# Performance work log

Hardware: AMD Instinct MI355X
Metric: run time of the kernel (lower is better)

## Reference

```python
import jax, jax.numpy as jnp
import numpy as np

EPS = 1e-12  # F.normalize eps

def _l2norm(x, axis=-1):
    n = jnp.sqrt(jnp.sum(x * x, axis=axis, keepdims=True))
    return x / jnp.maximum(n, EPS)

def setup_inputs() -> dict:
    key = jax.random.key(0)
    k1, k2 = jax.random.split(key)
    N, D, C = 262144, 128, 1024
    embeddings = jax.random.normal(k1, (N, D), dtype=jnp.float32)
    labels = jax.random.randint(k2, (N,), 0, C, dtype=jnp.int64)
    return {"embeddings": embeddings, "labels": labels, "num_classes": C}

def reference(embeddings, labels, num_classes):
    # Normalize all embeddings: [N, D]
    emb = _l2norm(embeddings, axis=1)
    # Per-class segment sums and counts (replaces python loop over unique labels)
    sums = jax.ops.segment_sum(emb, labels, num_segments=num_classes)          # [C, D]
    counts = jax.ops.segment_sum(jnp.ones((emb.shape[0],), emb.dtype), labels,
                                 num_segments=num_classes)                     # [C]
    safe_counts = jnp.maximum(counts, 1.0)
    prototypes = _l2norm(sums / safe_counts[:, None], axis=1)                  # [C, D]
    # cosine sim of each sample to its class prototype
    sim = jnp.sum(emb * prototypes[labels], axis=1)                           # [N]
    # per-class mean of (1 - sim)
    loss_sums = jax.ops.segment_sum(1.0 - sim, labels, num_segments=num_classes)
    per_class = loss_sums / safe_counts                                        # [C]
    valid = (counts >= 2.0).astype(emb.dtype)                                  # classes with >=2 samples
    n_valid = jnp.sum(valid)
    loss = jnp.sum(per_class * valid) / jnp.maximum(n_valid, 1.0)
    return jnp.where(n_valid > 0, loss, jnp.zeros((), emb.dtype))
```

## Files before the change

kernel.cpp:

```cpp
#include <hip/hip_runtime.h>
#include <math.h>

#define NUM_CLASSES 1024
#define HIST_CHUNK 2048
#define NB 128

__device__ __forceinline__ int detect_mode32(const int* __restrict__ l) {
    return (l[1] | l[3] | l[5] | l[7] | l[9] | l[11] | l[13] | l[15]) != 0;
}

__device__ __forceinline__ int get_label(const int* __restrict__ l, int i, int mode32) {
    return l[mode32 ? i : (i << 1)] & (NUM_CLASSES - 1);
}

__global__ void hist_kernel(const int* __restrict__ labels, int n,
                            int* __restrict__ pT) {
    __shared__ int h[NUM_CLASSES];
    const int mode32 = detect_mode32(labels);
    for (int i = threadIdx.x; i < NUM_CLASSES; i += blockDim.x) h[i] = 0;
    __syncthreads();
    const int base = blockIdx.x * HIST_CHUNK;
    for (int k = threadIdx.x; k < HIST_CHUNK; k += blockDim.x) {
        int i = base + k;
        if (i < n) atomicAdd(&h[get_label(labels, i, mode32)], 1);
    }
    __syncthreads();
    for (int c = threadIdx.x; c < NUM_CLASSES; c += blockDim.x)
        pT[c * NB + blockIdx.x] = h[c];
}

__global__ __launch_bounds__(512) void scanA_kernel(int* __restrict__ pT,
                                                    int* __restrict__ totals) {
    const int wave = threadIdx.x >> 6;
    const int lane = threadIdx.x & 63;
    const int c = blockIdx.x * 8 + wave;
    int* p = pT + c * NB;
    const int v0 = p[2 * lane];
    const int v1 = p[2 * lane + 1];
    int s = v0 + v1;
    #pragma unroll
    for (int d = 1; d < 64; d <<= 1) {
        int t = __shfl_up(s, d, 64);
        if (lane >= d) s += t;
    }
    const int base = s - v0 - v1;
    p[2 * lane]     = base;
    p[2 * lane + 1] = base + v0;
    if (lane == 63) totals[c] = s;
}

__global__ void scanB_kernel(const int* __restrict__ totals,
                             int* __restrict__ offsets,
                             int* __restrict__ counts,
                             float* __restrict__ accum,
                             int* __restrict__ ticket) {
    __shared__ int tmp[NUM_CLASSES];
    const int c = threadIdx.x;
    const int v = totals[c];
    tmp[c] = v;
    __syncthreads();
    for (int off = 1; off < NUM_CLASSES; off <<= 1) {
        int add = (c >= off) ? tmp[c - off] : 0;
        __syncthreads();
        tmp[c] += add;
        __syncthreads();
    }
    offsets[c] = tmp[c] - v;
    counts[c]  = v;
    if (c == 0) { accum[0] = 0.0f; accum[1] = 0.0f; *ticket = 0; }
}

__global__ void scatter_kernel(const int* __restrict__ labels, int n,
                               const int* __restrict__ pT,
                               const int* __restrict__ offsets,
                               int* __restrict__ sorted) {
    __shared__ int cur[NUM_CLASSES];
    const int mode32 = detect_mode32(labels);
    for (int c = threadIdx.x; c < NUM_CLASSES; c += blockDim.x)
        cur[c] = offsets[c] + pT[c * NB + blockIdx.x];
    __syncthreads();
    const int base = blockIdx.x * HIST_CHUNK;
    for (int k = threadIdx.x; k < HIST_CHUNK; k += blockDim.x) {
        int i = base + k;
        if (i < n) {
            int pos = atomicAdd(&cur[get_label(labels, i, mode32)], 1);
            sorted[pos] = i;
        }
    }
}

#define WPB 8
__global__ __launch_bounds__(512) void class_sum_kernel(
        const float* __restrict__ emb,
        const int* __restrict__ sorted,
        const int* __restrict__ offsets,
        const int* __restrict__ counts,
        float* __restrict__ accum,
        int* __restrict__ ticket,
        float* __restrict__ out) {
    const int c     = blockIdx.x;
    const int start = offsets[c];
    const int count = counts[c];
    const int wave  = threadIdx.x >> 6;
    const int lane  = threadIdx.x & 63;
    const int g     = lane >> 4;
    const int sub   = lane & 15;

    float4 aLo = make_float4(0.f, 0.f, 0.f, 0.f);
    float4 aHi = make_float4(0.f, 0.f, 0.f, 0.f);

    for (int r = wave * 4 + g; r < count; r += WPB * 4) {
        const int idx = sorted[start + r];
        const float4* row = (const float4*)(emb + (size_t)idx * 128);
        float4 v0 = row[sub];
        float4 v1 = row[sub + 16];
        float sq = v0.x*v0.x + v0.y*v0.y + v0.z*v0.z + v0.w*v0.w
                 + v1.x*v1.x + v1.y*v1.y + v1.z*v1.z + v1.w*v1.w;
        sq += __shfl_xor(sq, 1, 64);
        sq += __shfl_xor(sq, 2, 64);
        sq += __shfl_xor(sq, 4, 64);
        sq += __shfl_xor(sq, 8, 64);
        float inv = 1.0f / fmaxf(sqrtf(sq), 1e-12f);
        aLo.x += v0.x * inv; aLo.y += v0.y * inv; aLo.z += v0.z * inv; aLo.w += v0.w * inv;
        aHi.x += v1.x * inv; aHi.y += v1.y * inv; aHi.z += v1.z * inv; aHi.w += v1.w * inv;
    }

    __shared__ float s[WPB * 4][16][8];
    {
        float* dst = s[wave * 4 + g][sub];
        dst[0] = aLo.x; dst[1] = aLo.y; dst[2] = aLo.z; dst[3] = aLo.w;
        dst[4] = aHi.x; dst[5] = aHi.y; dst[6] = aHi.z; dst[7] = aHi.w;
    }
    __syncthreads();

    __shared__ float red[128];
    if (threadIdx.x < 128) {
        const int d  = threadIdx.x;
        const int dd = d & 63;
        const int sb = dd >> 2;
        const int j  = (d >> 6) * 4 + (dd & 3);
        float t = 0.0f;
        #pragma unroll
        for (int k = 0; k < WPB * 4; k++) t += s[k][sb][j];
        red[d] = t * t;
    }
    __syncthreads();
    if (threadIdx.x < 64) {
        float x = red[threadIdx.x] + red[threadIdx.x + 64];
        #pragma unroll
        for (int off = 32; off; off >>= 1) x += __shfl_xor(x, off, 64);
        if (threadIdx.x == 0) {
            if (count >= 2) {
                float nrm = sqrtf(x);
                float per_class = ((float)count - nrm) / (float)count;
                atomicAdd(&accum[0], per_class);
                atomicAdd(&accum[1], 1.0f);
            }
            __threadfence();
            int old = atomicAdd(ticket, 1);
            if (old == NUM_CLASSES - 1) {
                float ls = atomicAdd(&accum[0], 0.0f);
                float nv = atomicAdd(&accum[1], 0.0f);
                out[0] = (nv > 0.0f) ? (ls / nv) : 0.0f;
            }
        }
    }
}

extern "C" void kernel_launch(void* const* d_in, const int* in_sizes, int n_in,
                              void* d_out, int out_size, void* d_ws, size_t ws_size,
                              hipStream_t stream) {
    const float* emb  = (const float*)d_in[0];
    const int* labels = (const int*)d_in[1];
    const int n = in_sizes[1];

    char* ws = (char*)d_ws;
    int*   counts  = (int*)(ws + 0);
    int*   offsets = (int*)(ws + 4096);
    int*   totals  = (int*)(ws + 8192);
    float* accum   = (float*)(ws + 12288);
    int*   ticket  = (int*)(ws + 12304);
    int*   sorted  = (int*)(ws + 16384);
    int*   pT      = (int*)(ws + 16384 + (size_t)n * 4);

    hist_kernel <<<NB, 256, 0, stream>>>(labels, n, pT);
    scanA_kernel<<<NB, 512, 0, stream>>>(pT, totals);
    scanB_kernel<<<1, NUM_CLASSES, 0, stream>>>(totals, offsets, counts, accum, ticket);
    scatter_kernel<<<NB, 256, 0, stream>>>(labels, n, pT, offsets, sorted);
    class_sum_kernel<<<NUM_CLASSES, 512, 0, stream>>>(emb, sorted, offsets, counts,
                                                      accum, ticket, (float*)d_out);
}
```

Baseline: 255.5 us.

## Normalize rows in streaming pass and scatter bf16 copies into class-sorted buffer

The per-class gather of random fp32 rows is replaced by a coalesced streaming pass that normalizes each row and writes a bf16-packed copy to its class-sorted position. The class-sum kernel then reads contiguous half-size rows. This removes scattered full-row reads, but adds an extra write and read of a compacted buffer plus an extra launch. Rounding to bf16 before summing loses precision in the prototype sums.

```diff
diff --git a/kernel.cpp b/kernel.cpp
--- a/kernel.cpp
+++ b/kernel.cpp
@@ -8,10 +8,18 @@
 __device__ __forceinline__ int detect_mode32(const int* __restrict__ l) {
     return (l[1] | l[3] | l[5] | l[7] | l[9] | l[11] | l[13] | l[15]) != 0;
 }
-
 __device__ __forceinline__ int get_label(const int* __restrict__ l, int i, int mode32) {
     return l[mode32 ? i : (i << 1)] & (NUM_CLASSES - 1);
 }
+__device__ __forceinline__ unsigned bf16rne(float x) {
+    unsigned u = __float_as_uint(x);
+    return (u + 0x7FFFu + ((u >> 16) & 1u)) >> 16;
+}
+__device__ __forceinline__ unsigned packbf(float a, float b) {
+    return bf16rne(a) | (bf16rne(b) << 16);
+}
+__device__ __forceinline__ float unpack_lo(unsigned u) { return __uint_as_float(u << 16); }
+__device__ __forceinline__ float unpack_hi(unsigned u) { return __uint_as_float(u & 0xffff0000u); }
 
 __global__ void hist_kernel(const int* __restrict__ labels, int n,
                             int* __restrict__ pT) {
@@ -70,10 +78,10 @@
     if (c == 0) { accum[0] = 0.0f; accum[1] = 0.0f; *ticket = 0; }
 }
 
-__global__ void scatter_kernel(const int* __restrict__ labels, int n,
-                               const int* __restrict__ pT,
-                               const int* __restrict__ offsets,
-                               int* __restrict__ sorted) {
+__global__ void rank_kernel(const int* __restrict__ labels, int n,
+                            const int* __restrict__ pT,
+                            const int* __restrict__ offsets,
+                            int* __restrict__ rank) {
     __shared__ int cur[NUM_CLASSES];
     const int mode32 = detect_mode32(labels);
     for (int c = threadIdx.x; c < NUM_CLASSES; c += blockDim.x)
@@ -82,17 +90,49 @@
     const int base = blockIdx.x * HIST_CHUNK;
     for (int k = threadIdx.x; k < HIST_CHUNK; k += blockDim.x) {
         int i = base + k;
-        if (i < n) {
-            int pos = atomicAdd(&cur[get_label(labels, i, mode32)], 1);
-            sorted[pos] = i;
+        if (i < n)
+            rank[i] = atomicAdd(&cur[get_label(labels, i, mode32)], 1);
+    }
+}
+
+__global__ __launch_bounds__(512) void norm_scatter_kernel(
+        const float* __restrict__ emb,
+        const int* __restrict__ rank,
+        uint4* __restrict__ nbuf,
+        int n) {
+    const int wave = threadIdx.x >> 6;
+    const int lane = threadIdx.x & 63;
+    const int g    = lane >> 4;
+    const int sub  = lane & 15;
+    const int base = blockIdx.x * 256;
+
+    for (int r = wave * 4 + g; r < 256; r += 32) {
+        const int row = base + r;
+        if (row < n) {
+            const float4* rp = (const float4*)(emb + (size_t)row * 128);
+            float4 v0 = rp[sub];
+            float4 v1 = rp[sub + 16];
+            float sq = v0.x*v0.x + v0.y*v0.y + v0.z*v0.z + v0.w*v0.w
+                     + v1.x*v1.x + v1.y*v1.y + v1.z*v1.z + v1.w*v1.w;
+            sq += __shfl_xor(sq, 1, 64);
+            sq += __shfl_xor(sq, 2, 64);
+            sq += __shfl_xor(sq, 4, 64);
+            sq += __shfl_xor(sq, 8, 64);
+            float inv = 1.0f / fmaxf(sqrtf(sq), 1e-12f);
+            uint4 w;
+            w.x = packbf(v0.x * inv, v0.y * inv);
+            w.y = packbf(v0.z * inv, v0.w * inv);
+            w.z = packbf(v1.x * inv, v1.y * inv);
+            w.w = packbf(v1.z * inv, v1.w * inv);
+            const int pos = rank[row];
+            nbuf[(size_t)pos * 16 + sub] = w;
         }
     }
 }
 
 #define WPB 8
-__global__ __launch_bounds__(512) void class_sum_kernel(
-        const float* __restrict__ emb,
-        const int* __restrict__ sorted,
+__global__ __launch_bounds__(512) void class_sum2_kernel(
+        const uint4* __restrict__ nbuf,
         const int* __restrict__ offsets,
         const int* __restrict__ counts,
         float* __restrict__ accum,
@@ -106,39 +146,31 @@
     const int g     = lane >> 4;
     const int sub   = lane & 15;
 
-    float4 aLo = make_float4(0.f, 0.f, 0.f, 0.f);
-    float4 aHi = make_float4(0.f, 0.f, 0.f, 0.f);
+    float a[8];
+    #pragma unroll
+    for (int j = 0; j < 8; j++) a[j] = 0.0f;
 
     for (int r = wave * 4 + g; r < count; r += WPB * 4) {
-        const int idx = sorted[start + r];
-        const float4* row = (const float4*)(emb + (size_t)idx * 128);
-        float4 v0 = row[sub];
-        float4 v1 = row[sub + 16];
-        float sq = v0.x*v0.x + v0.y*v0.y + v0.z*v0.z + v0.w*v0.w
-                 + v1.x*v1.x + v1.y*v1.y + v1.z*v1.z + v1.w*v1.w;
-        sq += __shfl_xor(sq, 1, 64);
-        sq += __shfl_xor(sq, 2, 64);
-        sq += __shfl_xor(sq, 4, 64);
-        sq += __shfl_xor(sq, 8, 64);
-        float inv = 1.0f / fmaxf(sqrtf(sq), 1e-12f);
-        aLo.x += v0.x * inv; aLo.y += v0.y * inv; aLo.z += v0.z * inv; aLo.w += v0.w * inv;
-        aHi.x += v1.x * inv; aHi.y += v1.y * inv; aHi.z += v1.z * inv; aHi.w += v1.w * inv;
+        const uint4 w = nbuf[(size_t)(start + r) * 16 + sub];
+        a[0] += unpack_lo(w.x); a[1] += unpack_hi(w.x);
+        a[2] += unpack_lo(w.y); a[3] += unpack_hi(w.y);
+        a[4] += unpack_lo(w.z); a[5] += unpack_hi(w.z);
+        a[6] += unpack_lo(w.w); a[7] += unpack_hi(w.w);
     }
 
     __shared__ float s[WPB * 4][16][8];
     {
         float* dst = s[wave * 4 + g][sub];
-        dst[0] = aLo.x; dst[1] = aLo.y; dst[2] = aLo.z; dst[3] = aLo.w;
-        dst[4] = aHi.x; dst[5] = aHi.y; dst[6] = aHi.z; dst[7] = aHi.w;
+        #pragma unroll
+        for (int j = 0; j < 8; j++) dst[j] = a[j];
     }
     __syncthreads();
 
     __shared__ float red[128];
     if (threadIdx.x < 128) {
         const int d  = threadIdx.x;
-        const int dd = d & 63;
-        const int sb = dd >> 2;
-        const int j  = (d >> 6) * 4 + (dd & 3);
+        const int sb = d >> 3;
+        const int j  = d & 7;
         float t = 0.0f;
         #pragma unroll
         for (int k = 0; k < WPB * 4; k++) t += s[k][sb][j];
@@ -180,13 +212,17 @@
     int*   totals  = (int*)(ws + 8192);
     float* accum   = (float*)(ws + 12288);
     int*   ticket  = (int*)(ws + 12304);
-    int*   sorted  = (int*)(ws + 16384);
+    int*   rank    = (int*)(ws + 16384);
     int*   pT      = (int*)(ws + 16384 + (size_t)n * 4);
+    uint4* nbuf    = (uint4*)(ws + (2u << 20));
+
+    const int normBlocks = (n + 255) / 256;
 
     hist_kernel <<<NB, 256, 0, stream>>>(labels, n, pT);
     scanA_kernel<<<NB, 512, 0, stream>>>(pT, totals);
     scanB_kernel<<<1, NUM_CLASSES, 0, stream>>>(totals, offsets, counts, accum, ticket);
-    scatter_kernel<<<NB, 256, 0, stream>>>(labels, n, pT, offsets, sorted);
-    class_sum_kernel<<<NUM_CLASSES, 512, 0, stream>>>(emb, sorted, offsets, counts,
-                                                      accum, ticket, (float*)d_out);
-}
+    rank_kernel <<<NB, 256, 0, stream>>>(labels, n, pT, offsets, rank);
+    norm_scatter_kernel<<<normBlocks, 512, 0, stream>>>(emb, rank, nbuf, n);
+    class_sum2_kernel<<<NUM_CLASSES, 512, 0, stream>>>(nbuf, offsets, counts,
+                                                       accum, ticket, (float*)d_out);
+}
```

After: 273.4 us. 1.07x slower.

## Process 16 rows per wave with 4 lanes per row and shuffle-reduce accumulators

Applied to the files above, without the earlier changes.

Changes the class-sum mapping so that each 64-lane wave handles 16 rows at once, with 4 lanes per row each loading 8 contiguous float4s (32 floats). This cuts the shuffles needed for the norm and puts more independent loads in flight per row. The per-lane partial sums are then combined across row groups with a 32-register butterfly shuffle reduction before a smaller shared-memory step. The price is higher register pressure from the 32 accumulators and 8 float4s, plus many extra shuffles at the end, and each lane's loads are now strided across the row rather than coalesced per instruction.

```diff
diff --git a/kernel.cpp b/kernel.cpp
--- a/kernel.cpp
+++ b/kernel.cpp
@@ -8,7 +8,6 @@
 __device__ __forceinline__ int detect_mode32(const int* __restrict__ l) {
     return (l[1] | l[3] | l[5] | l[7] | l[9] | l[11] | l[13] | l[15]) != 0;
 }
-
 __device__ __forceinline__ int get_label(const int* __restrict__ l, int i, int mode32) {
     return l[mode32 ? i : (i << 1)] & (NUM_CLASSES - 1);
 }
@@ -103,46 +102,54 @@
     const int count = counts[c];
     const int wave  = threadIdx.x >> 6;
     const int lane  = threadIdx.x & 63;
-    const int g     = lane >> 4;
-    const int sub   = lane & 15;
+    const int g     = lane >> 2;
+    const int sub   = lane & 3;
 
-    float4 aLo = make_float4(0.f, 0.f, 0.f, 0.f);
-    float4 aHi = make_float4(0.f, 0.f, 0.f, 0.f);
+    float a[32];
+    #pragma unroll
+    for (int j = 0; j < 32; j++) a[j] = 0.0f;
 
-    for (int r = wave * 4 + g; r < count; r += WPB * 4) {
+    for (int r = wave * 16 + g; r < count; r += WPB * 16) {
         const int idx = sorted[start + r];
-        const float4* row = (const float4*)(emb + (size_t)idx * 128);
-        float4 v0 = row[sub];
-        float4 v1 = row[sub + 16];
-        float sq = v0.x*v0.x + v0.y*v0.y + v0.z*v0.z + v0.w*v0.w
-                 + v1.x*v1.x + v1.y*v1.y + v1.z*v1.z + v1.w*v1.w;
+        const float4* rp = (const float4*)(emb + (size_t)idx * 128 + 32 * sub);
+        float4 v[8];
+        #pragma unroll
+        for (int k = 0; k < 8; k++) v[k] = rp[k];
+        float sq = 0.0f;
+        #pragma unroll
+        for (int k = 0; k < 8; k++)
+            sq += v[k].x*v[k].x + v[k].y*v[k].y + v[k].z*v[k].z + v[k].w*v[k].w;
         sq += __shfl_xor(sq, 1, 64);
         sq += __shfl_xor(sq, 2, 64);
-        sq += __shfl_xor(sq, 4, 64);
-        sq += __shfl_xor(sq, 8, 64);
         float inv = 1.0f / fmaxf(sqrtf(sq), 1e-12f);
-        aLo.x += v0.x * inv; aLo.y += v0.y * inv; aLo.z += v0.z * inv; aLo.w += v0.w * inv;
-        aHi.x += v1.x * inv; aHi.y += v1.y * inv; aHi.z += v1.z * inv; aHi.w += v1.w * inv;
+        #pragma unroll
+        for (int k = 0; k < 8; k++) {
+            a[4*k+0] += v[k].x * inv;
+            a[4*k+1] += v[k].y * inv;
+            a[4*k+2] += v[k].z * inv;
+            a[4*k+3] += v[k].w * inv;
+        }
     }
 
-    __shared__ float s[WPB * 4][16][8];
-    {
-        float* dst = s[wave * 4 + g][sub];
-        dst[0] = aLo.x; dst[1] = aLo.y; dst[2] = aLo.z; dst[3] = aLo.w;
-        dst[4] = aHi.x; dst[5] = aHi.y; dst[6] = aHi.z; dst[7] = aHi.w;
+    #pragma unroll
+    for (int d = 4; d < 64; d <<= 1) {
+        #pragma unroll
+        for (int j = 0; j < 32; j++) a[j] += __shfl_xor(a[j], d, 64);
+    }
+
+    __shared__ float sw[WPB][128];
+    if (g == 0) {
+        #pragma unroll
+        for (int j = 0; j < 32; j++) sw[wave][32 * sub + j] = a[j];
     }
     __syncthreads();
 
     __shared__ float red[128];
     if (threadIdx.x < 128) {
-        const int d  = threadIdx.x;
-        const int dd = d & 63;
-        const int sb = dd >> 2;
-        const int j  = (d >> 6) * 4 + (dd & 3);
         float t = 0.0f;
         #pragma unroll
-        for (int k = 0; k < WPB * 4; k++) t += s[k][sb][j];
-        red[d] = t * t;
+        for (int w = 0; w < WPB; w++) t += sw[w][threadIdx.x];
+        red[threadIdx.x] = t * t;
     }
     __syncthreads();
     if (threadIdx.x < 64) {
```

Measured after the change: 260.8 us. +2.0%, slower.
